# Kernel optimization log

Measured on AMD Instinct MI355X. Metric: run time of the kernel, lower is better.

The kernel has to match this reference:

```python
import jax, jax.numpy as jnp
import numpy as np

N_NODES = 100000
N_EDGES = 500000
H = 128
EPS = 1e-5


def _mlp(x, W1, b1, W2, b2, W3, b3, g, beta):
    # 3-layer MLP (ReLU) + final LayerNorm, matching build_mlp(..., lay_norm=True, n_layers=3)
    h = jax.nn.relu(x @ W1 + b1)
    h = jax.nn.relu(h @ W2 + b2)
    h = h @ W3 + b3
    mu = jnp.mean(h, axis=-1, keepdims=True)
    var = jnp.var(h, axis=-1, keepdims=True)
    return (h - mu) * jax.lax.rsqrt(var + EPS) * g + beta


def setup_inputs() -> dict:
    key = jax.random.key(0)
    ks = jax.random.split(key, 20)
    s = lambda fan_in: 1.0 / np.sqrt(fan_in)
    inp = {
        "x": jax.random.normal(ks[0], (N_NODES, H), dtype=jnp.float32),
        "edge_attr": jax.random.normal(ks[1], (N_EDGES, H), dtype=jnp.float32),
        "edge_index": jax.random.randint(ks[2], (2, N_EDGES), 0, N_NODES, dtype=jnp.int64),
        # Edge MLP: in = 3H
        "eW1": jax.random.normal(ks[3], (3 * H, H), dtype=jnp.float32) * s(3 * H),
        "eb1": jnp.zeros((H,), jnp.float32),
        "eW2": jax.random.normal(ks[4], (H, H), dtype=jnp.float32) * s(H),
        "eb2": jnp.zeros((H,), jnp.float32),
        "eW3": jax.random.normal(ks[5], (H, H), dtype=jnp.float32) * s(H),
        "eb3": jnp.zeros((H,), jnp.float32),
        "eg": jnp.ones((H,), jnp.float32),
        "ebeta": jnp.zeros((H,), jnp.float32),
        # Node MLP: in = 2H
        "nW1": jax.random.normal(ks[6], (2 * H, H), dtype=jnp.float32) * s(2 * H),
        "nb1": jnp.zeros((H,), jnp.float32),
        "nW2": jax.random.normal(ks[7], (H, H), dtype=jnp.float32) * s(H),
        "nb2": jnp.zeros((H,), jnp.float32),
        "nW3": jax.random.normal(ks[8], (H, H), dtype=jnp.float32) * s(H),
        "nb3": jnp.zeros((H,), jnp.float32),
        "ng": jnp.ones((H,), jnp.float32),
        "nbeta": jnp.zeros((H,), jnp.float32),
    }
    return inp


def reference(x, edge_attr, edge_index,
              eW1, eb1, eW2, eb2, eW3, eb3, eg, ebeta,
              nW1, nb1, nW2, nb2, nW3, nb3, ng, nbeta):
    senders = edge_index[0]
    receivers = edge_index[1]
    # EdgeBlock: gather src/dst node feats, concat with edge feats, MLP (3H -> H)
    e_in = jnp.concatenate([x[senders], x[receivers], edge_attr], axis=-1)
    e_new = _mlp(e_in, eW1, eb1, eW2, eb2, eW3, eb3, eg, ebeta)
    # NodeBlock: scatter-sum edge messages to receiver nodes, concat with node feats, MLP (2H -> H)
    agg = jax.ops.segment_sum(e_new, receivers, num_segments=N_NODES)
    n_in = jnp.concatenate([x, agg], axis=-1)
    x_new = _mlp(n_in, nW1, nb1, nW2, nb2, nW3, nb3, ng, nbeta)
    # Residual connections
    return (x + x_new, edge_attr + e_new)
```

## Files before the change

kernel.cpp:

```cpp
#include <hip/hip_runtime.h>

#define N_NODES 100000
#define N_EDGES 500000
#define H 128
#define EPS 1e-5f

typedef __attribute__((ext_vector_type(8))) short bf16x8;
typedef __attribute__((ext_vector_type(4))) float f32x4;

__device__ __forceinline__ unsigned short f2bf(float f) {
  unsigned int u = __builtin_bit_cast(unsigned int, f);
  u += 0x7FFFu + ((u >> 16) & 1u);
  return (unsigned short)(u >> 16);
}
__device__ __forceinline__ float bf2f(unsigned short u) {
  return __builtin_bit_cast(float, (unsigned)u << 16);
}

__device__ __forceinline__ int swz(int r, int k) {
  return r * 128 + (k ^ ((r & 7) << 3));
}

union PK8 { unsigned short u[8]; uint4 q; };

#define GLDS16(g, l)                                                        \
  __builtin_amdgcn_global_load_lds(                                         \
      (const __attribute__((address_space(1))) void*)(g),                   \
      (__attribute__((address_space(3))) void*)(l), 16, 0, 0)

__device__ __forceinline__ void stage_w512(unsigned short* dst,
                                           const unsigned short* img) {
  const int t = threadIdx.x;
  #pragma unroll
  for (int j = 0; j < 4; ++j)
    GLDS16((const char*)img + j * 8192 + t * 16, (char*)dst + j * 8192 + t * 16);
}

__device__ __forceinline__ void gemm_regA(const bf16x8 a[4], const unsigned short* Wb,
                                          int m0, int kq, f32x4 acc[8]) {
  #pragma unroll
  for (int kk = 0; kk < 4; ++kk) {
    const int k0 = kk * 32 + kq * 8;
    #pragma unroll
    for (int tc = 0; tc < 8; ++tc) {
      bf16x8 b = *(const bf16x8*)&Wb[swz(tc * 16 + m0, k0)];
      acc[tc] = __builtin_amdgcn_mfma_f32_16x16x32_bf16(a[kk], b, acc[tc], 0, 0, 0);
    }
  }
}

__device__ __forceinline__ void gemm_ldsA(const unsigned short* Hb, int wrow,
                                          const unsigned short* Wb,
                                          int m0, int kq, f32x4 acc[8]) {
  #pragma unroll
  for (int kk = 0; kk < 4; ++kk) {
    const int k0 = kk * 32 + kq * 8;
    bf16x8 a = *(const bf16x8*)&Hb[swz(wrow + m0, k0)];
    #pragma unroll
    for (int tc = 0; tc < 8; ++tc) {
      bf16x8 b = *(const bf16x8*)&Wb[swz(tc * 16 + m0, k0)];
      acc[tc] = __builtin_amdgcn_mfma_f32_16x16x32_bf16(a, b, acc[tc], 0, 0, 0);
    }
  }
}

__device__ __forceinline__ void zero_acc(f32x4 acc[8]) {
  #pragma unroll
  for (int b = 0; b < 8; ++b) acc[b] = (f32x4){0.f, 0.f, 0.f, 0.f};
}

__device__ __forceinline__ void write_h(unsigned short* Hb, const f32x4 acc[8],
                                        const float* __restrict__ bias,
                                        int wrow, int m0, int kq) {
  #pragma unroll
  for (int tc = 0; tc < 8; ++tc) {
    const int col = tc * 16 + m0;
    const float b = bias[col];
    #pragma unroll
    for (int i = 0; i < 4; ++i)
      Hb[swz(wrow + kq * 4 + i, col)] = f2bf(fmaxf(acc[tc][i] + b, 0.0f));
  }
}

__device__ __forceinline__ void ln4(const f32x4 acc[8], float mu[4], float rv[4]) {
  float s[4] = {0, 0, 0, 0}, ss[4] = {0, 0, 0, 0};
  #pragma unroll
  for (int tc = 0; tc < 8; ++tc)
    #pragma unroll
    for (int i = 0; i < 4; ++i) {
      const float v = acc[tc][i];
      s[i] += v;
      ss[i] += v * v;
    }
  #pragma unroll
  for (int off = 1; off < 16; off <<= 1)
    #pragma unroll
    for (int i = 0; i < 4; ++i) {
      s[i] += __shfl_xor(s[i], off);
      ss[i] += __shfl_xor(ss[i], off);
    }
  #pragma unroll
  for (int i = 0; i < 4; ++i) {
    const float m = s[i] * (1.0f / 128.0f);
    const float var = ss[i] * (1.0f / 128.0f) - m * m;
    mu[i] = m;
    rv[i] = rsqrtf(var + EPS);
  }
}


__global__ void xprep_kernel(const float* __restrict__ x,
                             unsigned short* __restrict__ xb) {
  const long i = (long)blockIdx.x * 256 + threadIdx.x;
  const long base = i * 8;
  if (base < (long)N_NODES * H) {
    float4 v0 = *(const float4*)(x + base);
    float4 v1 = *(const float4*)(x + base + 4);
    PK8 pk;
    pk.u[0] = f2bf(v0.x); pk.u[1] = f2bf(v0.y);
    pk.u[2] = f2bf(v0.z); pk.u[3] = f2bf(v0.w);
    pk.u[4] = f2bf(v1.x); pk.u[5] = f2bf(v1.y);
    pk.u[6] = f2bf(v1.z); pk.u[7] = f2bf(v1.w);
    *(uint4*)(xb + base) = pk.q;
  }
}

struct WSrc { const float* p[9]; };

__global__ void wprep_kernel(WSrc wsrc, unsigned short* __restrict__ wimg) {
  const int id = blockIdx.x * 256 + threadIdx.x;
  const int m = id >> 14;
  const int r = id & 16383;
  const int n = r & 127;
  const int k = r >> 7;
  wimg[m * 16384 + swz(n, k)] = f2bf(wsrc.p[m][k * 128 + n]);
}


__global__ void hist_kernel(const int* __restrict__ ridx, unsigned* __restrict__ cnt) {
  const int e = blockIdx.x * 256 + threadIdx.x;
  if (e < N_EDGES) atomicAdd(&cnt[ridx[e]], 1u);
}

__global__ void scan1_kernel(const unsigned* __restrict__ cnt,
                             unsigned* __restrict__ offs,
                             unsigned* __restrict__ part) {
  __shared__ unsigned sh[256];
  const int t = threadIdx.x;
  const int base = blockIdx.x * 1024 + t * 4;
  unsigned v[4];
  #pragma unroll
  for (int i = 0; i < 4; ++i) v[i] = (base + i < N_NODES) ? cnt[base + i] : 0u;
  unsigned pre[4];
  pre[0] = 0; pre[1] = v[0]; pre[2] = v[0] + v[1]; pre[3] = pre[2] + v[2];
  const unsigned tot = pre[3] + v[3];
  sh[t] = tot;
  __syncthreads();
  for (int d = 1; d < 256; d <<= 1) {
    const unsigned u_ = (t >= d) ? sh[t - d] : 0u;
    __syncthreads();
    sh[t] += u_;
    __syncthreads();
  }
  const unsigned excl = sh[t] - tot;
  #pragma unroll
  for (int i = 0; i < 4; ++i)
    if (base + i < N_NODES) offs[base + i] = excl + pre[i];
  if (t == 255) part[blockIdx.x] = sh[255];
}

__global__ void scan2_kernel(unsigned* __restrict__ part, int n) {
  __shared__ unsigned sh[128];
  const int t = threadIdx.x;
  const unsigned v = (t < n) ? part[t] : 0u;
  sh[t] = v;
  __syncthreads();
  for (int d = 1; d < 128; d <<= 1) {
    const unsigned u_ = (t >= d) ? sh[t - d] : 0u;
    __syncthreads();
    sh[t] += u_;
    __syncthreads();
  }
  if (t < n) part[t] = sh[t] - v;
}

__global__ void scan3_kernel(unsigned* __restrict__ offs,
                             const unsigned* __restrict__ part,
                             unsigned* __restrict__ cursor) {
  const int i = blockIdx.x * 256 + threadIdx.x;
  if (i < N_NODES) {
    const unsigned o = offs[i] + part[i >> 10];
    offs[i] = o;
    cursor[i] = o;
  }
  if (i == 0) offs[N_NODES] = N_EDGES;
}

__global__ void scatter_kernel(const int* __restrict__ ridx,
                               unsigned* __restrict__ cursor,
                               unsigned* __restrict__ eord) {
  const int e = blockIdx.x * 256 + threadIdx.x;
  if (e < N_EDGES) {
    const unsigned p = atomicAdd(&cursor[ridx[e]], 1u);
    eord[p] = (unsigned)e;
  }
}


__global__ __launch_bounds__(512, 4) void edge_kernel(
    const unsigned short* __restrict__ xb, const float* __restrict__ edge_attr,
    const int* __restrict__ eidx, const unsigned short* __restrict__ wimg,
    const float* __restrict__ eb1, const float* __restrict__ eb2,
    const float* __restrict__ eb3,
    const float* __restrict__ eg, const float* __restrict__ ebeta,
    float* __restrict__ out_e, unsigned short* __restrict__ enew) {
  __shared__ unsigned short Wbuf[128 * 128];
  __shared__ unsigned short Hbuf[128 * 128];

  const int t = threadIdx.x;
  const int lane = t & 63;
  const int wave = t >> 6;
  const int wrow = wave * 16;
  const int m0 = lane & 15;
  const int kq = lane >> 4;
  const long e0 = (long)blockIdx.x * 128;
  const int* sidx = eidx;
  const int* ridx = eidx + N_EDGES;

  stage_w512(Wbuf, wimg + 0L * 16384);
  stage_w512(Hbuf, wimg + 1L * 16384);

  long erow = e0 + wrow + m0;
  if (erow > N_EDGES - 1) erow = N_EDGES - 1;
  const long ns = sidx[erow];
  const long nr = ridx[erow];
  bf16x8 aS[4], aR[4];
  {
    const unsigned short* ps = xb + ns * H + kq * 8;
    const unsigned short* pr = xb + nr * H + kq * 8;
    #pragma unroll
    for (int kk = 0; kk < 4; ++kk) {
      aS[kk] = *(const bf16x8*)(ps + kk * 32);
      aR[kk] = *(const bf16x8*)(pr + kk * 32);
    }
  }

  f32x4 acc[8];
  zero_acc(acc);

  __syncthreads();
  gemm_regA(aS, Wbuf, m0, kq, acc);
  gemm_regA(aR, Hbuf, m0, kq, acc);

  bf16x8 aE[4];
  {
    const float* pe = edge_attr + erow * (long)H + kq * 8;
    #pragma unroll
    for (int kk = 0; kk < 4; ++kk) {
      float4 v0 = *(const float4*)(pe + kk * 32);
      float4 v1 = *(const float4*)(pe + kk * 32 + 4);
      PK8 pk;
      pk.u[0] = f2bf(v0.x); pk.u[1] = f2bf(v0.y);
      pk.u[2] = f2bf(v0.z); pk.u[3] = f2bf(v0.w);
      pk.u[4] = f2bf(v1.x); pk.u[5] = f2bf(v1.y);
      pk.u[6] = f2bf(v1.z); pk.u[7] = f2bf(v1.w);
      aE[kk] = __builtin_bit_cast(bf16x8, pk.q);
    }
  }

  __syncthreads();
  stage_w512(Wbuf, wimg + 2L * 16384);
  __syncthreads();
  gemm_regA(aE, Wbuf, m0, kq, acc);

  __syncthreads();
  stage_w512(Wbuf, wimg + 3L * 16384);
  write_h(Hbuf, acc, eb1, wrow, m0, kq);
  zero_acc(acc);
  __syncthreads();
  gemm_ldsA(Hbuf, wrow, Wbuf, m0, kq, acc);

  __syncthreads();
  stage_w512(Wbuf, wimg + 4L * 16384);
  write_h(Hbuf, acc, eb2, wrow, m0, kq);
  zero_acc(acc);
  __syncthreads();
  gemm_ldsA(Hbuf, wrow, Wbuf, m0, kq, acc);

  float gm[8], bt[8];
  #pragma unroll
  for (int tc = 0; tc < 8; ++tc) {
    const int col = tc * 16 + m0;
    const float b3 = eb3[col];
    gm[tc] = eg[col];
    bt[tc] = ebeta[col];
    #pragma unroll
    for (int i = 0; i < 4; ++i) acc[tc][i] += b3;
  }
  float mu[4], rv[4];
  ln4(acc, mu, rv);

  __syncthreads();
  #pragma unroll
  for (int tc = 0; tc < 8; ++tc) {
    const int col = tc * 16 + m0;
    #pragma unroll
    for (int i = 0; i < 4; ++i) {
      const float y = (acc[tc][i] - mu[i]) * rv[i] * gm[tc] + bt[tc];
      Hbuf[swz(wrow + kq * 4 + i, col)] = f2bf(y);
    }
  }
  __syncthreads();

  {
    const int r = t >> 2;
    const int c0 = (t & 3) * 32;
    const long e = e0 + r;
    if (e < N_EDGES) {
      const float* ea = edge_attr + e * (long)H + c0;
      float* oe = out_e + e * (long)H + c0;
      unsigned short* en = enew + e * (long)H + c0;
      #pragma unroll
      for (int c2 = 0; c2 < 4; ++c2) {
        uint4 qv = *(const uint4*)&Hbuf[swz(r, c0 + c2 * 8)];
        *(uint4*)(en + c2 * 8) = qv;
        const unsigned short* pu = (const unsigned short*)&qv;
        float4 a0 = *(const float4*)(ea + c2 * 8);
        float4 a1 = *(const float4*)(ea + c2 * 8 + 4);
        float4 o0, o1;
        o0.x = a0.x + bf2f(pu[0]); o0.y = a0.y + bf2f(pu[1]);
        o0.z = a0.z + bf2f(pu[2]); o0.w = a0.w + bf2f(pu[3]);
        o1.x = a1.x + bf2f(pu[4]); o1.y = a1.y + bf2f(pu[5]);
        o1.z = a1.z + bf2f(pu[6]); o1.w = a1.w + bf2f(pu[7]);
        *(float4*)(oe + c2 * 8) = o0;
        *(float4*)(oe + c2 * 8 + 4) = o1;
      }
    }
  }
}

__global__ __launch_bounds__(512, 4) void node_kernel(
    const unsigned short* __restrict__ xb, const float* __restrict__ x,
    const unsigned short* __restrict__ enew,
    const unsigned* __restrict__ offs, const unsigned* __restrict__ eord,
    const unsigned short* __restrict__ wimg,
    const float* __restrict__ nb1, const float* __restrict__ nb2,
    const float* __restrict__ nb3,
    const float* __restrict__ ng, const float* __restrict__ nbeta,
    float* __restrict__ out_x) {
  __shared__ unsigned short Wbuf[128 * 128];
  __shared__ unsigned short Hbuf[128 * 128];

  const int t = threadIdx.x;
  const int lane = t & 63;
  const int wave = t >> 6;
  const int wrow = wave * 16;
  const int m0 = lane & 15;
  const int kq = lane >> 4;
  const long n0 = (long)blockIdx.x * 128;

  stage_w512(Wbuf, wimg + 5L * 16384);

  long nrow = n0 + wrow + m0;
  if (nrow > N_NODES - 1) nrow = N_NODES - 1;
  bf16x8 aX[4];
  {
    const unsigned short* px = xb + nrow * H + kq * 8;
    #pragma unroll
    for (int kk = 0; kk < 4; ++kk) aX[kk] = *(const bf16x8*)(px + kk * 32);
  }

  float av[32];
  #pragma unroll
  for (int i = 0; i < 32; ++i) av[i] = 0.f;
  {
    const long sn = n0 + (t >> 2);
    if (sn < N_NODES) {
      const unsigned o0 = offs[sn], o1 = offs[sn + 1];
      const int c0 = (t & 3) * 32;
      for (unsigned u_ = o0; u_ < o1; ++u_) {
        const unsigned short* er = enew + (long)eord[u_] * H + c0;
        #pragma unroll
        for (int c2 = 0; c2 < 4; ++c2) {
          uint4 qv = *(const uint4*)(er + c2 * 8);
          const unsigned short* pu = (const unsigned short*)&qv;
          #pragma unroll
          for (int j = 0; j < 8; ++j) av[c2 * 8 + j] += bf2f(pu[j]);
        }
      }
    }
  }

  f32x4 acc[8];
  zero_acc(acc);

  __syncthreads();
  gemm_regA(aX, Wbuf, m0, kq, acc);
  __syncthreads();
  stage_w512(Wbuf, wimg + 6L * 16384);
  {
    const int r = t >> 2;
    const int c0 = (t & 3) * 32;
    #pragma unroll
    for (int c2 = 0; c2 < 4; ++c2) {
      PK8 pk;
      #pragma unroll
      for (int j = 0; j < 8; ++j) pk.u[j] = f2bf(av[c2 * 8 + j]);
      *(uint4*)&Hbuf[swz(r, c0 + c2 * 8)] = pk.q;
    }
  }
  __syncthreads();
  gemm_ldsA(Hbuf, wrow, Wbuf, m0, kq, acc);

  __syncthreads();
  stage_w512(Wbuf, wimg + 7L * 16384);
  write_h(Hbuf, acc, nb1, wrow, m0, kq);
  zero_acc(acc);
  __syncthreads();
  gemm_ldsA(Hbuf, wrow, Wbuf, m0, kq, acc);

  __syncthreads();
  stage_w512(Wbuf, wimg + 8L * 16384);
  write_h(Hbuf, acc, nb2, wrow, m0, kq);
  zero_acc(acc);
  __syncthreads();
  gemm_ldsA(Hbuf, wrow, Wbuf, m0, kq, acc);

  float gm[8], bt[8];
  #pragma unroll
  for (int tc = 0; tc < 8; ++tc) {
    const int col = tc * 16 + m0;
    const float b3 = nb3[col];
    gm[tc] = ng[col];
    bt[tc] = nbeta[col];
    #pragma unroll
    for (int i = 0; i < 4; ++i) acc[tc][i] += b3;
  }
  float mu[4], rv[4];
  ln4(acc, mu, rv);

  __syncthreads();
  #pragma unroll
  for (int tc = 0; tc < 8; ++tc) {
    const int col = tc * 16 + m0;
    #pragma unroll
    for (int i = 0; i < 4; ++i) {
      const float y = (acc[tc][i] - mu[i]) * rv[i] * gm[tc] + bt[tc];
      Hbuf[swz(wrow + kq * 4 + i, col)] = f2bf(y);
    }
  }
  __syncthreads();

  {
    const int r = t >> 2;
    const int c0 = (t & 3) * 32;
    const long n = n0 + r;
    if (n < N_NODES) {
      const float* xr = x + n * (long)H + c0;
      float* ox = out_x + n * (long)H + c0;
      #pragma unroll
      for (int c2 = 0; c2 < 4; ++c2) {
        uint4 qv = *(const uint4*)&Hbuf[swz(r, c0 + c2 * 8)];
        const unsigned short* pu = (const unsigned short*)&qv;
        float4 a0 = *(const float4*)(xr + c2 * 8);
        float4 a1 = *(const float4*)(xr + c2 * 8 + 4);
        float4 o0, o1;
        o0.x = a0.x + bf2f(pu[0]); o0.y = a0.y + bf2f(pu[1]);
        o0.z = a0.z + bf2f(pu[2]); o0.w = a0.w + bf2f(pu[3]);
        o1.x = a1.x + bf2f(pu[4]); o1.y = a1.y + bf2f(pu[5]);
        o1.z = a1.z + bf2f(pu[6]); o1.w = a1.w + bf2f(pu[7]);
        *(float4*)(ox + c2 * 8) = o0;
        *(float4*)(ox + c2 * 8 + 4) = o1;
      }
    }
  }
}

extern "C" void kernel_launch(void* const* d_in, const int* in_sizes, int n_in,
                              void* d_out, int out_size, void* d_ws, size_t ws_size,
                              hipStream_t stream) {
  (void)in_sizes; (void)n_in; (void)out_size; (void)ws_size;
  const float* x         = (const float*)d_in[0];
  const float* edge_attr = (const float*)d_in[1];
  const int*   eidx      = (const int*)d_in[2];
  const float* eW1 = (const float*)d_in[3];
  const float* eb1 = (const float*)d_in[4];
  const float* eW2 = (const float*)d_in[5];
  const float* eb2 = (const float*)d_in[6];
  const float* eW3 = (const float*)d_in[7];
  const float* eb3 = (const float*)d_in[8];
  const float* eg  = (const float*)d_in[9];
  const float* ebt = (const float*)d_in[10];
  const float* nW1 = (const float*)d_in[11];
  const float* nb1 = (const float*)d_in[12];
  const float* nW2 = (const float*)d_in[13];
  const float* nb2 = (const float*)d_in[14];
  const float* nW3 = (const float*)d_in[15];
  const float* nb3 = (const float*)d_in[16];
  const float* ng  = (const float*)d_in[17];
  const float* nbt = (const float*)d_in[18];

  float* out_x = (float*)d_out;
  float* out_e = (float*)d_out + (size_t)N_NODES * H;

  char* w = (char*)d_ws;
  unsigned short* enew = (unsigned short*)(w + 0);
  unsigned short* xb   = (unsigned short*)(w + 128000000);
  unsigned short* wimg = (unsigned short*)(w + 153600000);
  unsigned* offs   = (unsigned*)(w + 153894912);
  unsigned* cnt    = (unsigned*)(w + 154295040);
  unsigned* cursor = (unsigned*)(w + 154695168);
  unsigned* part   = (unsigned*)(w + 155095296);
  unsigned* eord   = (unsigned*)(w + 155096320);

  const int* ridx = eidx + N_EDGES;

  hipMemsetAsync(cnt, 0, (size_t)N_NODES * sizeof(unsigned), stream);

  WSrc wsrc;
  wsrc.p[0] = eW1;
  wsrc.p[1] = eW1 + 16384;
  wsrc.p[2] = eW1 + 32768;
  wsrc.p[3] = eW2;
  wsrc.p[4] = eW3;
  wsrc.p[5] = nW1;
  wsrc.p[6] = nW1 + 16384;
  wsrc.p[7] = nW2;
  wsrc.p[8] = nW3;

  xprep_kernel<<<(N_NODES * H / 8 + 255) / 256, 256, 0, stream>>>(x, xb);
  wprep_kernel<<<576, 256, 0, stream>>>(wsrc, wimg);

  hist_kernel<<<(N_EDGES + 255) / 256, 256, 0, stream>>>(ridx, cnt);
  scan1_kernel<<<(N_NODES + 1023) / 1024, 256, 0, stream>>>(cnt, offs, part);
  scan2_kernel<<<1, 128, 0, stream>>>(part, (N_NODES + 1023) / 1024);
  scan3_kernel<<<(N_NODES + 255) / 256, 256, 0, stream>>>(offs, part, cursor);
  scatter_kernel<<<(N_EDGES + 255) / 256, 256, 0, stream>>>(ridx, cursor, eord);

  const int eblocks = (N_EDGES + 127) / 128;
  const int nblocks = (N_NODES + 127) / 128;
  edge_kernel<<<eblocks, 512, 0, stream>>>(xb, edge_attr, eidx, wimg, eb1, eb2, eb3,
                                           eg, ebt, out_e, enew);
  node_kernel<<<nblocks, 512, 0, stream>>>(xb, x, enew, offs, eord, wimg,
                                           nb1, nb2, nb3, ng, nbt, out_x);
}
```

Baseline: 459.0 us.

## Precompute per-node first-layer projections and gather them in edge kernel

Adds a node-level kernel that computes x·W1_sender (plus bias) and x·W1_receiver once per node and stores them as bf16. The edge kernel then gathers these projected rows per edge and adds them to the edge_attr GEMM result, instead of gathering raw node features and running two extra 128x128 GEMMs per edge. This cuts first-layer edge FLOPs by two thirds and removes two weight stagings per block. In exchange it adds an extra kernel, extra workspace, and a second bf16 rounding of the partial sums, which shifts numerics slightly.

New measurement: 455.8 us. No clear change (-0.7%).

```diff
diff --git a/kernel.cpp b/kernel.cpp
--- a/kernel.cpp
+++ b/kernel.cpp
@@ -79,6 +79,17 @@
     #pragma unroll
     for (int i = 0; i < 4; ++i)
       Hb[swz(wrow + kq * 4 + i, col)] = f2bf(fmaxf(acc[tc][i] + b, 0.0f));
+  }
+}
+
+__device__ __forceinline__ void write_h0(unsigned short* Hb, const f32x4 acc[8],
+                                         int wrow, int m0, int kq) {
+  #pragma unroll
+  for (int tc = 0; tc < 8; ++tc) {
+    const int col = tc * 16 + m0;
+    #pragma unroll
+    for (int i = 0; i < 4; ++i)
+      Hb[swz(wrow + kq * 4 + i, col)] = f2bf(fmaxf(acc[tc][i], 0.0f));
   }
 }
 
@@ -137,6 +148,71 @@
 }
 
 
+__global__ __launch_bounds__(512, 2) void px_kernel(
+    const float* __restrict__ x, const unsigned short* __restrict__ wimg,
+    const float* __restrict__ eb1,
+    unsigned short* __restrict__ pxs, unsigned short* __restrict__ pxr) {
+  __shared__ unsigned short smem[2 * 16384];
+  const int t = threadIdx.x;
+  #pragma unroll
+  for (int j = 0; j < 8; ++j)
+    GLDS16((const char*)wimg + j * 8192 + t * 16, (char*)smem + j * 8192 + t * 16);
+  __syncthreads();
+
+  const int lane = t & 63;
+  const int wtile = (t >> 6) * 16;
+  const int m0 = lane & 15;
+  const int kq = lane >> 4;
+  const long n0 = (long)blockIdx.x * 128;
+
+  long an = n0 + wtile + m0;
+  if (an > N_NODES - 1) an = N_NODES - 1;
+  const float* px_ = x + an * H + kq * 8;
+  bf16x8 aX[4];
+  #pragma unroll
+  for (int kk = 0; kk < 4; ++kk) {
+    float4 v0 = *(const float4*)(px_ + kk * 32);
+    float4 v1 = *(const float4*)(px_ + kk * 32 + 4);
+    PK8 pk;
+    pk.u[0] = f2bf(v0.x); pk.u[1] = f2bf(v0.y);
+    pk.u[2] = f2bf(v0.z); pk.u[3] = f2bf(v0.w);
+    pk.u[4] = f2bf(v1.x); pk.u[5] = f2bf(v1.y);
+    pk.u[6] = f2bf(v1.z); pk.u[7] = f2bf(v1.w);
+    aX[kk] = __builtin_bit_cast(bf16x8, pk.q);
+  }
+  const long cbn = n0 + wtile + kq * 4;
+
+  f32x4 acc[8];
+  float bv[8];
+  zero_acc(acc);
+  gemm_regA(aX, smem, m0, kq, acc);
+  #pragma unroll
+  for (int tc = 0; tc < 8; ++tc) bv[tc] = eb1[tc * 16 + m0];
+  #pragma unroll
+  for (int i = 0; i < 4; ++i) {
+    const long nn = cbn + i;
+    if (nn < N_NODES) {
+      PK8 pk;
+      #pragma unroll
+      for (int tc = 0; tc < 8; ++tc) pk.u[tc] = f2bf(acc[tc][i] + bv[tc]);
+      *(uint4*)(pxs + nn * H + m0 * 8) = pk.q;
+    }
+  }
+  zero_acc(acc);
+  gemm_regA(aX, smem + 16384, m0, kq, acc);
+  #pragma unroll
+  for (int i = 0; i < 4; ++i) {
+    const long nn = cbn + i;
+    if (nn < N_NODES) {
+      PK8 pk;
+      #pragma unroll
+      for (int tc = 0; tc < 8; ++tc) pk.u[tc] = f2bf(acc[tc][i]);
+      *(uint4*)(pxr + nn * H + m0 * 8) = pk.q;
+    }
+  }
+}
+
+
 __global__ void hist_kernel(const int* __restrict__ ridx, unsigned* __restrict__ cnt) {
   const int e = blockIdx.x * 256 + threadIdx.x;
   if (e < N_EDGES) atomicAdd(&cnt[ridx[e]], 1u);
@@ -208,10 +284,10 @@
 
 
 __global__ __launch_bounds__(512, 4) void edge_kernel(
-    const unsigned short* __restrict__ xb, const float* __restrict__ edge_attr,
-    const int* __restrict__ eidx, const unsigned short* __restrict__ wimg,
-    const float* __restrict__ eb1, const float* __restrict__ eb2,
-    const float* __restrict__ eb3,
+    const float* __restrict__ edge_attr, const int* __restrict__ eidx,
+    const unsigned short* __restrict__ wimg,
+    const unsigned short* __restrict__ pxs, const unsigned short* __restrict__ pxr,
+    const float* __restrict__ eb2, const float* __restrict__ eb3,
     const float* __restrict__ eg, const float* __restrict__ ebeta,
     float* __restrict__ out_e, unsigned short* __restrict__ enew) {
   __shared__ unsigned short Wbuf[128 * 128];
@@ -227,31 +303,23 @@
   const int* sidx = eidx;
   const int* ridx = eidx + N_EDGES;
 
-  stage_w512(Wbuf, wimg + 0L * 16384);
-  stage_w512(Hbuf, wimg + 1L * 16384);
+  stage_w512(Wbuf, wimg + 2L * 16384);
+
+  const long cb = e0 + wrow + kq * 4;
+  const long cbl = cb > (long)(N_EDGES - 4) ? (long)(N_EDGES - 4) : cb;
+  int4 s4 = *(const int4*)&sidx[cbl];
+  int4 r4 = *(const int4*)&ridx[cbl];
+  const int* sp = (const int*)&s4;
+  const int* rp = (const int*)&r4;
+  uint4 qs[4], qr[4];
+  #pragma unroll
+  for (int i = 0; i < 4; ++i) {
+    qs[i] = *(const uint4*)(pxs + (long)sp[i] * H + m0 * 8);
+    qr[i] = *(const uint4*)(pxr + (long)rp[i] * H + m0 * 8);
+  }
 
   long erow = e0 + wrow + m0;
   if (erow > N_EDGES - 1) erow = N_EDGES - 1;
-  const long ns = sidx[erow];
-  const long nr = ridx[erow];
-  bf16x8 aS[4], aR[4];
-  {
-    const unsigned short* ps = xb + ns * H + kq * 8;
-    const unsigned short* pr = xb + nr * H + kq * 8;
-    #pragma unroll
-    for (int kk = 0; kk < 4; ++kk) {
-      aS[kk] = *(const bf16x8*)(ps + kk * 32);
-      aR[kk] = *(const bf16x8*)(pr + kk * 32);
-    }
-  }
-
-  f32x4 acc[8];
-  zero_acc(acc);
-
-  __syncthreads();
-  gemm_regA(aS, Wbuf, m0, kq, acc);
-  gemm_regA(aR, Hbuf, m0, kq, acc);
-
   bf16x8 aE[4];
   {
     const float* pe = edge_attr + erow * (long)H + kq * 8;
@@ -268,14 +336,23 @@
     }
   }
 
-  __syncthreads();
-  stage_w512(Wbuf, wimg + 2L * 16384);
+  f32x4 acc[8];
+  zero_acc(acc);
+
   __syncthreads();
   gemm_regA(aE, Wbuf, m0, kq, acc);
+  #pragma unroll
+  for (int i = 0; i < 4; ++i) {
+    const unsigned short* us = (const unsigned short*)&qs[i];
+    const unsigned short* ur = (const unsigned short*)&qr[i];
+    #pragma unroll
+    for (int tc = 0; tc < 8; ++tc)
+      acc[tc][i] += bf2f(us[tc]) + bf2f(ur[tc]);
+  }
 
   __syncthreads();
   stage_w512(Wbuf, wimg + 3L * 16384);
-  write_h(Hbuf, acc, eb1, wrow, m0, kq);
+  write_h0(Hbuf, acc, wrow, m0, kq);
   zero_acc(acc);
   __syncthreads();
   gemm_ldsA(Hbuf, wrow, Wbuf, m0, kq, acc);
@@ -506,12 +583,14 @@
   char* w = (char*)d_ws;
   unsigned short* enew = (unsigned short*)(w + 0);
   unsigned short* xb   = (unsigned short*)(w + 128000000);
-  unsigned short* wimg = (unsigned short*)(w + 153600000);
-  unsigned* offs   = (unsigned*)(w + 153894912);
-  unsigned* cnt    = (unsigned*)(w + 154295040);
-  unsigned* cursor = (unsigned*)(w + 154695168);
-  unsigned* part   = (unsigned*)(w + 155095296);
-  unsigned* eord   = (unsigned*)(w + 155096320);
+  unsigned short* pxs  = (unsigned short*)(w + 153600000);
+  unsigned short* pxr  = (unsigned short*)(w + 179200000);
+  unsigned short* wimg = (unsigned short*)(w + 204800000);
+  unsigned* offs   = (unsigned*)(w + 205094912);
+  unsigned* cnt    = (unsigned*)(w + 205495040);
+  unsigned* cursor = (unsigned*)(w + 205895168);
+  unsigned* part   = (unsigned*)(w + 206295296);
+  unsigned* eord   = (unsigned*)(w + 206296320);
 
   const int* ridx = eidx + N_EDGES;
 
@@ -531,6 +610,8 @@
   xprep_kernel<<<(N_NODES * H / 8 + 255) / 256, 256, 0, stream>>>(x, xb);
   wprep_kernel<<<576, 256, 0, stream>>>(wsrc, wimg);
 
+  px_kernel<<<(N_NODES + 127) / 128, 512, 0, stream>>>(x, wimg, eb1, pxs, pxr);
+
   hist_kernel<<<(N_EDGES + 255) / 256, 256, 0, stream>>>(ridx, cnt);
   scan1_kernel<<<(N_NODES + 1023) / 1024, 256, 0, stream>>>(cnt, offs, part);
   scan2_kernel<<<1, 128, 0, stream>>>(part, (N_NODES + 1023) / 1024);
@@ -539,8 +620,8 @@
 
   const int eblocks = (N_EDGES + 127) / 128;
   const int nblocks = (N_NODES + 127) / 128;
-  edge_kernel<<<eblocks, 512, 0, stream>>>(xb, edge_attr, eidx, wimg, eb1, eb2, eb3,
-                                           eg, ebt, out_e, enew);
+  edge_kernel<<<eblocks, 512, 0, stream>>>(edge_attr, eidx, wimg, pxs, pxr,
+                                           eb2, eb3, eg, ebt, out_e, enew);
   node_kernel<<<nblocks, 512, 0, stream>>>(xb, x, enew, offs, eord, wimg,
                                            nb1, nb2, nb3, ng, nbt, out_x);
 }
```
